# Kernel tuning notes

Hardware: AMD Instinct MI355X
Metric: run time of the kernel (lower is better)

Reference implementation:

```python
import jax, jax.numpy as jnp
import numpy as np

HEAD_SIZE = 64
N_EMBD = 1024
B, T = 8, 4096

def setup_inputs() -> dict:
    key = jax.random.key(0)
    k1, k2, k3, k4 = jax.random.split(key, 4)
    x = jax.random.normal(k1, (B, T, N_EMBD), dtype=jnp.float32)
    # bias-free Linear weights, stored as [in, out] so y = x @ W
    scale = 1.0 / np.sqrt(N_EMBD)
    Wk = jax.random.uniform(k2, (N_EMBD, HEAD_SIZE), jnp.float32, -scale, scale)
    Wq = jax.random.uniform(k3, (N_EMBD, HEAD_SIZE), jnp.float32, -scale, scale)
    Wv = jax.random.uniform(k4, (N_EMBD, HEAD_SIZE), jnp.float32, -scale, scale)
    return {"x": x, "Wk": Wk, "Wq": Wq, "Wv": Wv}

def reference(x, Wk, Wq, Wv):
    # x: [B, T, C]
    k = x @ Wk  # [B, T, H]
    q = x @ Wq
    v = x @ Wv
    scale = HEAD_SIZE ** -0.5
    wei = jnp.einsum('bth,bsh->bts', q, k) * scale  # [B, T, T]
    Tn = x.shape[1]
    causal = jnp.tril(jnp.ones((Tn, Tn), dtype=bool))
    wei = jnp.where(causal, wei, -jnp.inf)
    wei = jax.nn.softmax(wei, axis=-1)
    # dropout p=0.0 -> identity (eval behavior)
    out = jnp.einsum('bts,bsh->bth', wei, v)  # [B, T, H]
    return out
```

## Files before the change

kernel.cpp:

```cpp
#include <hip/hip_runtime.h>
#include <hip/hip_bf16.h>


#define HS 64
#define NE 1024
#define NB 8
#define TS 4096
#define NROW (NB * TS)

#define QKV_BUF 20480
#define QKV_XB  12288

typedef __attribute__((ext_vector_type(4)))  float f32x4;
typedef __attribute__((ext_vector_type(16))) float f32x16;
typedef __attribute__((ext_vector_type(8)))  short s16x8;
typedef __attribute__((ext_vector_type(4)))  float vfloat4;

__device__ __forceinline__ unsigned short f2bf(float x) {
  return __builtin_bit_cast(unsigned short, __float2bfloat16(x));
}
__device__ __forceinline__ unsigned pkbf(float lo, float hi) {
  return (unsigned)f2bf(lo) | ((unsigned)f2bf(hi) << 16);
}

union ABFrag { s16x8 v; unsigned d[4]; };

__device__ __forceinline__ void gl_lds16(const void* g, const unsigned char* l) {
  __builtin_amdgcn_global_load_lds(
      (const __attribute__((address_space(1))) unsigned int*)(g),
      (__attribute__((address_space(3))) unsigned int*)(l), 16, 0, 0);
}

__global__ __launch_bounds__(256) void wt_kernel(const float* __restrict__ Wk,
                                                 const float* __restrict__ Wq,
                                                 const float* __restrict__ Wv,
                                                 unsigned short* __restrict__ wT2) {
  int gid = blockIdx.x * 256 + threadIdx.x;
  int j = gid & 7;
  int t1 = gid >> 3;
  int sk = t1 % 768;
  int c  = t1 / 768;
  int g = sk / 192, n = sk % 192;
  int k = c * 32 + g * 8 + j;
  const float* W = (n < 64) ? Wq : (n < 128) ? Wk : Wv;
  float s = (n < 64) ? 0.18033688011112042f : 1.0f;
  wT2[gid] = f2bf(W[k * 64 + (n & 63)] * s);
}

__global__ __launch_bounds__(256, 4) void qkv_kernel(const float* __restrict__ x,
                                                     const unsigned short* __restrict__ wT2,
                                                     unsigned short* __restrict__ q_ws,
                                                     unsigned short* __restrict__ kf,
                                                     unsigned short* __restrict__ vf) {
  __shared__ __align__(16) unsigned char smem[2 * QKV_BUF];
  const int t = threadIdx.x;
  const int w = t >> 6, lane = t & 63;
  const int g = lane >> 4, nn = lane & 15;
  const int m0blk = blockIdx.x * 64;
  const int m0 = m0blk + w * 16;

  f32x4 acc[12];
#pragma unroll
  for (int i = 0; i < 12; ++i) acc[i] = f32x4{0.f, 0.f, 0.f, 0.f};

  const unsigned short* wsrcA = wT2 + (size_t)(w * 192 + lane) * 8;
  const int wd0 = w * 3072;
  const float* xs0 = x + (size_t)(m0blk + w * 16 + 0 + (lane >> 3)) * NE + (lane & 7) * 4;
  const float* xs1 = x + (size_t)(m0blk + w * 16 + 8 + (lane >> 3)) * NE + (lane & 7) * 4;
  const int xd0 = QKV_XB + w * 2048;
  const int xd1 = xd0 + 1024;

  const int abase = QKV_XB + (w * 16 + nn) * 128 + g * 32;
  const int wbase = (g * 192 + nn) * 16;

#define ISSUE(C)                                                               \
  {                                                                            \
    unsigned char* db_ = smem + ((C) & 1) * QKV_BUF;                           \
    gl_lds16(wsrcA + (size_t)(C) * 6144, db_ + wd0);                           \
    gl_lds16(wsrcA + (size_t)(C) * 6144 + 512, db_ + wd0 + 1024);              \
    gl_lds16(wsrcA + (size_t)(C) * 6144 + 1024, db_ + wd0 + 2048);             \
    gl_lds16(xs0 + (C) * 32, db_ + xd0);                                       \
    gl_lds16(xs1 + (C) * 32, db_ + xd1);                                       \
  }

  ISSUE(0)
  __builtin_amdgcn_sched_barrier(0);
  ISSUE(1)
  __builtin_amdgcn_sched_barrier(0);

#define PHASE(C, VM, DOISS)                                                    \
  {                                                                            \
    asm volatile("s_waitcnt vmcnt(" #VM ")" ::: "memory");                     \
    __builtin_amdgcn_s_barrier();                                              \
    __builtin_amdgcn_sched_barrier(0);                                         \
    const unsigned char* bb_ = smem + ((C) & 1) * QKV_BUF;                     \
    const vfloat4 a0_ = *(const vfloat4*)(bb_ + abase);                        \
    const vfloat4 a1_ = *(const vfloat4*)(bb_ + abase + 16);                   \
    ABFrag af;                                                                 \
    af.d[0] = pkbf(a0_.x, a0_.y); af.d[1] = pkbf(a0_.z, a0_.w);                \
    af.d[2] = pkbf(a1_.x, a1_.y); af.d[3] = pkbf(a1_.z, a1_.w);                \
    _Pragma("unroll")                                                          \
    for (int i = 0; i < 12; ++i) {                                             \
      const s16x8 bf = *(const s16x8*)(bb_ + wbase + i * 256);                 \
      acc[i] = __builtin_amdgcn_mfma_f32_16x16x32_bf16(af.v, bf, acc[i], 0, 0, 0); \
    }                                                                          \
    __builtin_amdgcn_sched_barrier(0);                                         \
    __builtin_amdgcn_s_barrier();                                              \
    __builtin_amdgcn_sched_barrier(0);                                         \
    if (DOISS) { ISSUE((C) + 2) }                                              \
    __builtin_amdgcn_sched_barrier(0);                                         \
  }

#pragma unroll
  for (int c = 0; c < 30; ++c) PHASE(c, 5, 1)
  PHASE(30, 5, 0)
  PHASE(31, 0, 0)
#undef PHASE
#undef ISSUE

  const int rbase = m0 + 4 * g;
#pragma unroll
  for (int i = 0; i < 12; ++i) {
    const int c = 16 * i + nn;
#pragma unroll
    for (int j = 0; j < 4; ++j) {
      const int rr = rbase + j;
      const unsigned short hval = f2bf(acc[i][j]);
      const int b = rr >> 12, tt = rr & 4095;
      if (c < 64) {
        q_ws[(size_t)rr * HS + c] = hval;
      } else if (c < 128) {
        const int h = c - 64;
        const size_t idx = (size_t)b * 262144 + (size_t)(tt >> 5) * 2048 +
                           (h >> 4) * 512 + ((h >> 3) & 1) * 256 +
                           (tt & 31) * 8 + (h & 7);
        kf[idx] = hval;
      } else {
        const int h = c - 128;
        const size_t idx = (size_t)b * 262144 + (size_t)(tt >> 5) * 2048 +
                           (h >> 5) * 1024 + ((tt >> 4) & 1) * 512 +
                           ((tt >> 3) & 1) * 256 + (h & 31) * 8 + (tt & 7);
        vf[idx] = hval;
      }
    }
  }
}

#define TILE32F(DIAG, KF, VF, QF, L_RUN, O)                                    \
  {                                                                            \
    f32x16 st_;                                                                \
    _Pragma("unroll") for (int r = 0; r < 16; ++r) st_[r] = 0.f;               \
    __builtin_amdgcn_s_setprio(1);                                             \
    st_ = __builtin_amdgcn_mfma_f32_32x32x16_bf16(KF[0], QF[0], st_, 0, 0, 0); \
    st_ = __builtin_amdgcn_mfma_f32_32x32x16_bf16(KF[1], QF[1], st_, 0, 0, 0); \
    st_ = __builtin_amdgcn_mfma_f32_32x32x16_bf16(KF[2], QF[2], st_, 0, 0, 0); \
    st_ = __builtin_amdgcn_mfma_f32_32x32x16_bf16(KF[3], QF[3], st_, 0, 0, 0); \
    __builtin_amdgcn_s_setprio(0);                                             \
    if (DIAG) {                                                                \
      _Pragma("unroll") for (int r = 0; r < 16; ++r) {                         \
        const int kvl_ = (r & 3) + 8 * (r >> 2) + hi4;                         \
        if (kvl_ > qi) st_[r] = -1e30f;                                        \
      }                                                                        \
    }                                                                          \
    float p_[16];                                                              \
    _Pragma("unroll") for (int r = 0; r < 16; ++r)                             \
      p_[r] = __builtin_amdgcn_exp2f(st_[r]);                                  \
    float sm_ = ((p_[0] + p_[1]) + (p_[2] + p_[3])) +                          \
                ((p_[4] + p_[5]) + (p_[6] + p_[7]));                           \
    sm_ += ((p_[8] + p_[9]) + (p_[10] + p_[11])) +                             \
           ((p_[12] + p_[13]) + (p_[14] + p_[15]));                            \
    L_RUN += sm_;                                                              \
    const unsigned q01_ = pkbf(p_[0], p_[1]),   q23_ = pkbf(p_[2], p_[3]);     \
    const unsigned q45_ = pkbf(p_[4], p_[5]),   q67_ = pkbf(p_[6], p_[7]);     \
    const unsigned q89_ = pkbf(p_[8], p_[9]),   qab_ = pkbf(p_[10], p_[11]);   \
    const unsigned qcd_ = pkbf(p_[12], p_[13]), qef_ = pkbf(p_[14], p_[15]);   \
    const unsigned e0_ = (unsigned)__shfl_xor((int)(hi ? q01_ : q45_), 32, 64);\
    const unsigned e1_ = (unsigned)__shfl_xor((int)(hi ? q23_ : q67_), 32, 64);\
    const unsigned e2_ = (unsigned)__shfl_xor((int)(hi ? q89_ : qcd_), 32, 64);\
    const unsigned e3_ = (unsigned)__shfl_xor((int)(hi ? qab_ : qef_), 32, 64);\
    ABFrag pf0_, pf1_;                                                         \
    pf0_.d[0] = hi ? e0_ : q01_;                                               \
    pf0_.d[1] = hi ? e1_ : q23_;                                               \
    pf0_.d[2] = hi ? q45_ : e0_;                                               \
    pf0_.d[3] = hi ? q67_ : e1_;                                               \
    pf1_.d[0] = hi ? e2_ : q89_;                                               \
    pf1_.d[1] = hi ? e3_ : qab_;                                               \
    pf1_.d[2] = hi ? qcd_ : e2_;                                               \
    pf1_.d[3] = hi ? qef_ : e3_;                                               \
    __builtin_amdgcn_s_setprio(1);                                             \
    O[0] = __builtin_amdgcn_mfma_f32_32x32x16_bf16(VF[0], pf0_.v, O[0], 0,0,0);\
    O[0] = __builtin_amdgcn_mfma_f32_32x32x16_bf16(VF[1], pf1_.v, O[0], 0,0,0);\
    O[1] = __builtin_amdgcn_mfma_f32_32x32x16_bf16(VF[2], pf0_.v, O[1], 0,0,0);\
    O[1] = __builtin_amdgcn_mfma_f32_32x32x16_bf16(VF[3], pf1_.v, O[1], 0,0,0);\
    __builtin_amdgcn_s_setprio(0);                                             \
  }

#define LD4(dst, base)                                                         \
  dst[0] = *(const s16x8*)(base);                                              \
  dst[1] = *(const s16x8*)((base) + 512);                                      \
  dst[2] = *(const s16x8*)((base) + 1024);                                     \
  dst[3] = *(const s16x8*)((base) + 1536);

__global__ __launch_bounds__(512, 4) void attn_kernel(const unsigned short* __restrict__ q_ws,
                                                      const unsigned short* __restrict__ kf,
                                                      const unsigned short* __restrict__ vf,
                                                      float* __restrict__ out) {
  __shared__ float o_sm[2][4][16][68];
  __shared__ float l_sm[2][4][32];

  const int wv = threadIdx.x >> 6, lane = threadIdx.x & 63;
  const int qi = lane & 31, hi = lane >> 5;
  const int hi8 = 8 * hi, hi4 = 4 * hi;

  const int bid = blockIdx.x;
  const int b = bid & 7;
  const int pr = bid >> 3;
  const int tile = wv >> 2;
  const int wq = wv & 3;
  const int ti_x = tile ? (127 - pr) : pr;
  const int t0 = ti_x * 32;
  const int nt = ti_x + 1;

  const unsigned short* kfb = kf + (size_t)b * 262144 + lane * 8;
  const unsigned short* vfb = vf + (size_t)b * 262144 + lane * 8;
  const unsigned short* qr = q_ws + (size_t)(b * TS + t0 + qi) * HS + hi8;

  s16x8 qf[4];
#pragma unroll
  for (int kk = 0; kk < 4; ++kk) qf[kk] = *(const s16x8*)(qr + 16 * kk);

  f32x16 o[2];
#pragma unroll
  for (int r = 0; r < 16; ++r) { o[0][r] = 0.f; o[1][r] = 0.f; }
  float l_run = 0.f;

  for (int it = wq; it < nt; it += 4) {
    s16x8 kfr[4], vfr[4];
    LD4(kfr, kfb + (size_t)it * 2048)
    LD4(vfr, vfb + (size_t)it * 2048)
    TILE32F(it == ti_x, kfr, vfr, qf, l_run, o)
  }

  l_run += __shfl_xor(l_run, 32, 64);

  if (lane < 32) l_sm[tile][wq][lane] = l_run;
  const int X = threadIdx.x >> 8;
  const int rem = threadIdx.x & 255;
  const int q8m = rem >> 4;
  const int h0 = (rem & 15) * 4;
  const int t0X = (X ? (127 - pr) : pr) * 32;

#pragma unroll
  for (int P = 0; P < 2; ++P) {
    if ((qi >> 4) == P) {
      const int qr_ = qi & 15;
#pragma unroll
      for (int ht = 0; ht < 2; ++ht)
#pragma unroll
        for (int r = 0; r < 16; ++r) {
          const int h = ht * 32 + (r & 3) + 8 * (r >> 2) + hi4;
          o_sm[tile][wq][qr_][h] = o[ht][r];
        }
    }
    __syncthreads();
    {
      const int q = 16 * P + q8m;
      const float L = l_sm[X][0][q] + l_sm[X][1][q] +
                      l_sm[X][2][q] + l_sm[X][3][q];
      const float inv = 1.0f / L;
      float rv[4];
#pragma unroll
      for (int j = 0; j < 4; ++j)
        rv[j] = (o_sm[X][0][q8m][h0 + j] + o_sm[X][1][q8m][h0 + j] +
                 o_sm[X][2][q8m][h0 + j] + o_sm[X][3][q8m][h0 + j]) * inv;
      *(float4*)(out + ((size_t)(b * TS + t0X + q)) * HS + h0) =
          float4{rv[0], rv[1], rv[2], rv[3]};
    }
    if (P == 0) __syncthreads();
  }
}

extern "C" void kernel_launch(void* const* d_in, const int* in_sizes, int n_in,
                              void* d_out, int out_size, void* d_ws, size_t ws_size,
                              hipStream_t stream) {
  const float* x  = (const float*)d_in[0];
  const float* Wk = (const float*)d_in[1];
  const float* Wq = (const float*)d_in[2];
  const float* Wv = (const float*)d_in[3];
  float* out = (float*)d_out;

  unsigned short* wT2  = (unsigned short*)d_ws;
  unsigned short* q_ws = wT2 + 192 * 1024;
  unsigned short* kf   = q_ws + (size_t)NROW * HS;
  unsigned short* vf   = kf + (size_t)NROW * HS;

  wt_kernel<<<dim3(768), dim3(256), 0, stream>>>(Wk, Wq, Wv, wT2);
  qkv_kernel<<<dim3(NROW / 64), dim3(256), 0, stream>>>(x, wT2, q_ws, kf, vf);
  attn_kernel<<<dim3(512), dim3(512), 0, stream>>>(q_ws, kf, vf, out);
}
```

Before: 61.42 us.

## Process two 32-row query tiles per wave to reuse K/V loads

Each block now handles two 64-row query strips (one from each end of the causal triangle). Every wave covers both 32-row sub-tiles, so each K/V fragment load feeds two tiles, and waves are split between the strips in proportion to their work. This halves the grid to 256 blocks and lowers launch bounds to 2 blocks per CU because of the extra accumulator registers. The cost is more register pressure, fewer blocks to hide latency, and a longer cross-wave reduction with extra syncs.

New measurement: 65.04 us. +5.9%, slower.

```diff
diff --git a/kernel.cpp b/kernel.cpp
--- a/kernel.cpp
+++ b/kernel.cpp
@@ -201,12 +201,12 @@
   dst[2] = *(const s16x8*)((base) + 1024);                                     \
   dst[3] = *(const s16x8*)((base) + 1536);
 
-__global__ __launch_bounds__(512, 4) void attn_kernel(const unsigned short* __restrict__ q_ws,
+__global__ __launch_bounds__(512, 2) void attn_kernel(const unsigned short* __restrict__ q_ws,
                                                       const unsigned short* __restrict__ kf,
                                                       const unsigned short* __restrict__ vf,
                                                       float* __restrict__ out) {
-  __shared__ float o_sm[2][4][16][68];
-  __shared__ float l_sm[2][4][32];
+  __shared__ float o_sm[8][16][68];
+  __shared__ float l_sm[8][64];
 
   const int wv = threadIdx.x >> 6, lane = threadIdx.x & 63;
   const int qi = lane & 31, hi = lane >> 5;
@@ -215,68 +215,88 @@
   const int bid = blockIdx.x;
   const int b = bid & 7;
   const int pr = bid >> 3;
-  const int tile = wv >> 2;
-  const int wq = wv & 3;
-  const int ti_x = tile ? (127 - pr) : pr;
-  const int t0 = ti_x * 32;
-  const int nt = ti_x + 1;
+  const int ntA = 2 * pr + 2;
+  int wA = (8 * ntA + 65) / 130;
+  if (wA < 1) wA = 1;
+  if (wA > 7) wA = 7;
+
+  const int tile = (wv < wA) ? 0 : 1;
+  const int sidx = tile ? (wv - wA) : wv;
+  const int stride = tile ? (8 - wA) : wA;
+  const int sX = tile ? (63 - pr) : pr;
+  const int t0 = sX * 64;
+  const int ta = 2 * sX, tb = ta + 1;
+  const int nt = tb + 1;
 
   const unsigned short* kfb = kf + (size_t)b * 262144 + lane * 8;
   const unsigned short* vfb = vf + (size_t)b * 262144 + lane * 8;
-  const unsigned short* qr = q_ws + (size_t)(b * TS + t0 + qi) * HS + hi8;
-
-  s16x8 qf[4];
-#pragma unroll
-  for (int kk = 0; kk < 4; ++kk) qf[kk] = *(const s16x8*)(qr + 16 * kk);
-
-  f32x16 o[2];
-#pragma unroll
-  for (int r = 0; r < 16; ++r) { o[0][r] = 0.f; o[1][r] = 0.f; }
-  float l_run = 0.f;
-
-  for (int it = wq; it < nt; it += 4) {
+  const unsigned short* qra = q_ws + (size_t)(b * TS + t0 + qi) * HS + hi8;
+  const unsigned short* qrb = q_ws + (size_t)(b * TS + t0 + 32 + qi) * HS + hi8;
+
+  s16x8 qfa[4], qfb_[4];
+#pragma unroll
+  for (int kk = 0; kk < 4; ++kk) {
+    qfa[kk]  = *(const s16x8*)(qra + 16 * kk);
+    qfb_[kk] = *(const s16x8*)(qrb + 16 * kk);
+  }
+
+  f32x16 oa[2], ob[2];
+#pragma unroll
+  for (int r = 0; r < 16; ++r) { oa[0][r] = 0.f; oa[1][r] = 0.f; ob[0][r] = 0.f; ob[1][r] = 0.f; }
+  float la = 0.f, lb = 0.f;
+
+  for (int it = sidx; it < nt; it += stride) {
     s16x8 kfr[4], vfr[4];
     LD4(kfr, kfb + (size_t)it * 2048)
     LD4(vfr, vfb + (size_t)it * 2048)
-    TILE32F(it == ti_x, kfr, vfr, qf, l_run, o)
-  }
-
-  l_run += __shfl_xor(l_run, 32, 64);
-
-  if (lane < 32) l_sm[tile][wq][lane] = l_run;
+    if (it <= ta) TILE32F(it == ta, kfr, vfr, qfa, la, oa)
+    TILE32F(it == tb, kfr, vfr, qfb_, lb, ob)
+  }
+
+  la += __shfl_xor(la, 32, 64);
+  lb += __shfl_xor(lb, 32, 64);
+  if (lane < 32) { l_sm[wv][lane] = la; l_sm[wv][32 + lane] = lb; }
+
   const int X = threadIdx.x >> 8;
   const int rem = threadIdx.x & 255;
   const int q8m = rem >> 4;
   const int h0 = (rem & 15) * 4;
-  const int t0X = (X ? (127 - pr) : pr) * 32;
-
-#pragma unroll
-  for (int P = 0; P < 2; ++P) {
-    if ((qi >> 4) == P) {
-      const int qr_ = qi & 15;
-#pragma unroll
-      for (int ht = 0; ht < 2; ++ht)
-#pragma unroll
-        for (int r = 0; r < 16; ++r) {
-          const int h = ht * 32 + (r & 3) + 8 * (r >> 2) + hi4;
-          o_sm[tile][wq][qr_][h] = o[ht][r];
+  const int t0X = (X ? (63 - pr) : pr) * 64;
+
+#pragma unroll
+  for (int sub = 0; sub < 2; ++sub) {
+#pragma unroll
+    for (int P = 0; P < 2; ++P) {
+      if ((qi >> 4) == P) {
+        const int qr_ = qi & 15;
+#pragma unroll
+        for (int ht = 0; ht < 2; ++ht)
+#pragma unroll
+          for (int r = 0; r < 16; ++r) {
+            const int h = ht * 32 + (r & 3) + 8 * (r >> 2) + hi4;
+            o_sm[wv][qr_][h] = sub ? ob[ht][r] : oa[ht][r];
+          }
+      }
+      __syncthreads();
+      {
+        const int qrow = sub * 32 + 16 * P + q8m;
+        float L = 0.f;
+        float rv[4] = {0.f, 0.f, 0.f, 0.f};
+#pragma unroll
+        for (int w = 0; w < 8; ++w) {
+          const bool in = X ? (w >= wA) : (w < wA);
+          if (in) {
+            L += l_sm[w][qrow];
+#pragma unroll
+            for (int j = 0; j < 4; ++j) rv[j] += o_sm[w][q8m][h0 + j];
+          }
         }
+        const float inv = 1.0f / L;
+        *(float4*)(out + ((size_t)(b * TS + t0X + qrow)) * HS + h0) =
+            float4{rv[0] * inv, rv[1] * inv, rv[2] * inv, rv[3] * inv};
+      }
+      if (!(sub == 1 && P == 1)) __syncthreads();
     }
-    __syncthreads();
-    {
-      const int q = 16 * P + q8m;
-      const float L = l_sm[X][0][q] + l_sm[X][1][q] +
-                      l_sm[X][2][q] + l_sm[X][3][q];
-      const float inv = 1.0f / L;
-      float rv[4];
-#pragma unroll
-      for (int j = 0; j < 4; ++j)
-        rv[j] = (o_sm[X][0][q8m][h0 + j] + o_sm[X][1][q8m][h0 + j] +
-                 o_sm[X][2][q8m][h0 + j] + o_sm[X][3][q8m][h0 + j]) * inv;
-      *(float4*)(out + ((size_t)(b * TS + t0X + q)) * HS + h0) =
-          float4{rv[0], rv[1], rv[2], rv[3]};
-    }
-    if (P == 0) __syncthreads();
   }
 }
 
@@ -296,5 +316,5 @@
 
   wt_kernel<<<dim3(768), dim3(256), 0, stream>>>(Wk, Wq, Wv, wT2);
   qkv_kernel<<<dim3(NROW / 64), dim3(256), 0, stream>>>(x, wT2, q_ws, kf, vf);
-  attn_kernel<<<dim3(512), dim3(512), 0, stream>>>(q_ws, kf, vf, out);
-}
+  attn_kernel<<<dim3(256), dim3(512), 0, stream>>>(q_ws, kf, vf, out);
+}
```
